# Optimization experiments

Hardware: AMD Instinct MI355X
Metric: run time of the kernel (lower is better)

The kernel has to match this reference:

```python
import jax, jax.numpy as jnp
import numpy as np

BN_INV = 1.0 / np.float32(np.sqrt(1.0 + 1e-5))  # eval BN with running_mean=0, running_var=1


def _conv(x, w, stride):
    return jax.lax.conv_general_dilated(
        x, w, (stride, stride), [(1, 1), (1, 1)],
        dimension_numbers=('NCHW', 'OIHW', 'NCHW'))


def _se(x, w1, b1, w2, b2):
    # squeeze-excite: global avg pool -> fc -> relu -> fc -> sigmoid -> scale
    y = x.mean(axis=(2, 3))                       # (B, C)
    y = jax.nn.relu(y @ w1.T + b1)
    y = jax.nn.sigmoid(y @ w2.T + b2)
    return x * y[:, :, None, None]


def _squash(s):
    n2 = jnp.sum(s * s, axis=-1, keepdims=True)
    n = jnp.sqrt(n2)
    return s * (n2 / (1.0 + n2)) / (n + 1e-8)


def _block(x, cw, g, b, s1w, s1b, s2w, s2b, stride):
    h = _conv(x, cw, stride)
    h = h * (g * BN_INV)[None, :, None, None] + b[None, :, None, None]
    h = jax.nn.relu(h)
    return _se(h, s1w, s1b, s2w, s2b)


def setup_inputs() -> dict:
    key = jax.random.key(0)
    ks = jax.random.split(key, 32)
    rn = lambda i, shape, s=1.0: s * jax.random.normal(ks[i], shape, dtype=jnp.float32)
    d = {}
    d['x'] = rn(0, (64, 1, 128, 128))
    # feature extractor
    d['conv1_w'] = rn(1, (16, 1, 3, 3), 0.3)
    d['bn1_g'] = 1.0 + rn(2, (16,), 0.1)
    d['bn1_b'] = rn(3, (16,), 0.1)
    d['se1_w1'] = rn(4, (1, 16), 0.2); d['se1_b1'] = rn(5, (1,), 0.1)
    d['se1_w2'] = rn(6, (16, 1), 0.2); d['se1_b2'] = rn(7, (16,), 0.1)
    d['conv2_w'] = rn(8, (32, 16, 3, 3), 0.1)
    d['bn2_g'] = 1.0 + rn(9, (32,), 0.1)
    d['bn2_b'] = rn(10, (32,), 0.1)
    d['se2_w1'] = rn(11, (2, 32), 0.2); d['se2_b1'] = rn(12, (2,), 0.1)
    d['se2_w2'] = rn(13, (32, 2), 0.2); d['se2_b2'] = rn(14, (32,), 0.1)
    d['conv3_w'] = rn(15, (64, 32, 3, 3), 0.07)
    d['bn3_g'] = 1.0 + rn(16, (64,), 0.1)
    d['bn3_b'] = rn(17, (64,), 0.1)
    d['se3_w1'] = rn(18, (4, 64), 0.15); d['se3_b1'] = rn(19, (4,), 0.1)
    d['se3_w2'] = rn(20, (64, 4), 0.15); d['se3_b2'] = rn(21, (64,), 0.1)
    # primary capsules conv: 64 -> 8 caps * 8 dim = 64 channels, stride 2
    d['pc_w'] = rn(22, (64, 64, 3, 3), 0.05)
    d['pc_b'] = rn(23, (64,), 0.05)
    # digit capsule transform: (1, 2048, 3, 16, 8)
    d['W_digit'] = 0.01 * jax.random.normal(ks[24], (1, 2048, 3, 16, 8), dtype=jnp.float32)
    return d


def reference(x, conv1_w, bn1_g, bn1_b, se1_w1, se1_b1, se1_w2, se1_b2,
              conv2_w, bn2_g, bn2_b, se2_w1, se2_b1, se2_w2, se2_b2,
              conv3_w, bn3_g, bn3_b, se3_w1, se3_b1, se3_w2, se3_b2,
              pc_w, pc_b, W_digit):
    h = _block(x, conv1_w, bn1_g, bn1_b, se1_w1, se1_b1, se1_w2, se1_b2, 1)
    h = _block(h, conv2_w, bn2_g, bn2_b, se2_w1, se2_b1, se2_w2, se2_b2, 2)
    h = _block(h, conv3_w, bn3_g, bn3_b, se3_w1, se3_b1, se3_w2, se3_b2, 2)
    # primary capsules: conv -> (B, 8 caps, 8 dim, 16*16) -> (B, 2048, 8)
    u = _conv(h, pc_w, 2) + pc_b[None, :, None, None]     # (B, 64, 16, 16)
    B = u.shape[0]
    u = u.reshape(B, 8, 8, -1).transpose(0, 1, 3, 2).reshape(B, -1, 8)
    u = _squash(u)                                        # (B, 2048, 8)
    # u_hat[b,i,c,d] = sum_e W[0,i,c,d,e] * u[b,i,e]  (avoids torch's W.repeat)
    u_hat = jnp.einsum('icde,bie->bicd', W_digit[0], u)   # (B, 2048, 3, 16)
    b_ij = jnp.zeros((B, u_hat.shape[1], u_hat.shape[2], 1), u_hat.dtype)
    v_j = None
    for _ in range(3):  # fixed routing iterations
        c_ij = jax.nn.softmax(b_ij, axis=2)
        s_j = jnp.sum(c_ij * u_hat, axis=1, keepdims=True)  # (B,1,3,16)
        v_j = _squash(s_j)
        b_ij = b_ij + jnp.sum(u_hat * v_j, axis=-1, keepdims=True)
    v = v_j[:, 0]                                          # (B, 3, 16)
    return jnp.sqrt(jnp.sum(v * v, axis=-1))               # (B, 3) class lengths
```

## Files before the change

### kernel.cpp

```cpp
#include <hip/hip_runtime.h>
#include <math.h>

#define BN_INV_F 0.9999950000374997f

__device__ __forceinline__ void gload_lds4(const float* g, float* l) {
    __builtin_amdgcn_global_load_lds(
        (const __attribute__((address_space(1))) void*)g,
        (__attribute__((address_space(3))) void*)l, 4, 0, 0);
}
__device__ __forceinline__ void gload_lds16(const float* g, float* l) {
    __builtin_amdgcn_global_load_lds(
        (const __attribute__((address_space(1))) void*)g,
        (__attribute__((address_space(3))) void*)l, 16, 0, 0);
}

__global__ __launch_bounds__(256) void wtrans_all_k(
    const float* __restrict__ w1, const float* __restrict__ w2,
    const float* __restrict__ w3, const float* __restrict__ wp,
    float* __restrict__ w1t, float* __restrict__ w2t,
    float* __restrict__ w3t, float* __restrict__ wpt)
{
    int i = blockIdx.x * 256 + threadIdx.x;
    if (i < 144) {
        int co = i % 16, k = i / 16;
        w1t[i] = w1[co * 9 + k];
    } else if (i < 4752) {
        int t = i - 144;
        int co = t % 32, rk = t / 32, cin = rk / 9, k = rk % 9;
        w2t[t] = w2[(co * 16 + cin) * 9 + k];
    } else if (i < 23184) {
        int t = i - 4752;
        int co = t % 64, rk = t / 64, cin = rk / 9, k = rk % 9;
        w3t[t] = w3[(co * 32 + cin) * 9 + k];
    } else if (i < 60048) {
        int t = i - 23184;
        int co = t % 64, rk = t / 64, cin = rk / 9, k = rk % 9;
        wpt[t] = wp[(co * 64 + cin) * 9 + k];
    }
}

template <int CIN, int CINB, int COUT, int COB, int HIN, int HOUT, int STRIDE,
          int TW, int ROWS_T, int PPT, int CB, int NTHREADS,
          bool BN_RELU, bool SE_SUM, int HSE_IN, int KSPLIT>
__device__ __forceinline__ void conv_body(
    const float* __restrict__ in, const float* __restrict__ wt,
    const float* __restrict__ gamma, const float* __restrict__ beta,
    float* __restrict__ out, size_t pstride,
    float* __restrict__ se_sum, const float* __restrict__ se_sums_in,
    const float* __restrict__ se_w1, const float* __restrict__ se_b1,
    const float* __restrict__ se_w2, const float* __restrict__ se_b2,
    float inv_spatial)
{
    constexpr int WIN = HIN, WOUT = HOUT;
    constexpr int TH = ROWS_T * PPT;
    constexpr int IH_T = (TH - 1) * STRIDE + 3;
    constexpr int NW = NTHREADS / 64;
    constexpr int NCHUNK = CINB / CB;
    constexpr int SEGS = (WIN >= 64) ? (WIN / 64) : 1;
    constexpr int PAIRS = (IH_T + 1) / 2;
    constexpr int NG = COUT / COB;
    constexpr int IHW = IH_T * WIN;
    constexpr int CHUNK_BYTES = CB * IHW * 4;
    constexpr bool FAST16 = (CHUNK_BYTES % 1024) == 0;
    constexpr int NISS = CHUNK_BYTES / 1024;
    static_assert(NTHREADS == TW * ROWS_T, "geometry");
    static_assert(TW == WOUT, "tile must span full output width");
    static_assert(CINB % CB == 0, "chunking");
    static_assert(WIN % 64 == 0 || WIN == 32, "stage width");

    const int b = blockIdx.z;
    const int gy = blockIdx.y;
    const int ty = blockIdx.x;
    const int tid = threadIdx.x;
    const int wo = tid % TW;
    const int rg = tid / TW;
    const int g = gy % NG;
    const int kk = gy / NG;
    const int cin0 = kk * CINB;

    __shared__ float in_t[2][CB * IH_T * WIN];
    __shared__ float scl[CIN];
    __shared__ float gl[COB], bl[COB];
    __shared__ float red[NW][COB];
    __shared__ float hid[HSE_IN > 0 ? HSE_IN : 1];

    const float* inb = in + (size_t)b * CIN * HIN * WIN;
    const int gr0 = ty * TH * STRIDE - 1;
    const int wos = wo * STRIDE;
    const int wvid = tid >> 6, lane = tid & 63;
    const bool interior = (gr0 >= 0) && (gr0 + IH_T <= HIN);

    auto stage = [&](int c, int buf) {
        const int cb0 = cin0 + c * CB;
        float* bb = &in_t[buf][0];
        if (FAST16 && interior) {
            for (int i = wvid; i < NISS; i += NW) {
                int fe = i * 256 + lane * 4;
                int ci = fe / IHW;
                int rem = fe - ci * IHW;
                int lr = rem / WIN;
                int lc = rem - lr * WIN;
                const float* gsrc = inb + (size_t)(cb0 + ci) * (HIN * WIN)
                                  + (size_t)(gr0 + lr) * WIN + lc;
                gload_lds16(gsrc, bb + i * 256);
            }
        } else if (WIN >= 64) {
            for (int r = wvid; r < CB * IH_T; r += NW) {
                int ci = r / IH_T, lr = r - ci * IH_T;
                int gr = gr0 + lr;
                float* ldst = bb + (ci * IH_T + lr) * WIN;
                if (gr >= 0 && gr < HIN) {
                    const float* gsrc = inb + (size_t)(cb0 + ci) * HIN * WIN + (size_t)gr * WIN;
#pragma unroll
                    for (int s = 0; s < SEGS; ++s)
                        gload_lds4(gsrc + s * 64 + lane, ldst + s * 64);
                } else {
#pragma unroll
                    for (int s = 0; s < SEGS; ++s) ldst[s * 64 + lane] = 0.0f;
                }
            }
        } else {
            for (int pz = wvid; pz < CB * PAIRS; pz += NW) {
                int ci = pz / PAIRS, q = pz - ci * PAIRS;
                int lr0 = q * 2;
                int nr = (lr0 + 1 < IH_T) ? 2 : 1;
                int grr = gr0 + lr0;
                float* ldst = bb + (ci * IH_T + lr0) * WIN;
                if (nr == 2 && grr >= 0 && grr + 1 < HIN) {
                    const float* gsrc = inb + (size_t)(cb0 + ci) * HIN * WIN + (size_t)grr * WIN + lane;
                    gload_lds4(gsrc, ldst);
                } else {
                    for (int e = lane; e < nr * WIN; e += 64) {
                        int rr = e / WIN, cc = e - rr * WIN;
                        int gr = grr + rr;
                        ldst[e] = (gr >= 0 && gr < HIN)
                            ? inb[(size_t)(cb0 + ci) * HIN * WIN + (size_t)gr * WIN + cc] : 0.0f;
                    }
                }
            }
        }
    };

    stage(0, 0);

    if (HSE_IN > 0) {
        if (tid < HSE_IN) {
            float a = se_b1[tid];
            for (int c = 0; c < CIN; ++c)
                a = fmaf(se_sums_in[b * CIN + c] * inv_spatial, se_w1[tid * CIN + c], a);
            hid[tid] = fmaxf(a, 0.0f);
        }
        __syncthreads();
        if (tid < CIN) {
            float a = se_b2[tid];
            for (int h = 0; h < HSE_IN; ++h)
                a = fmaf(hid[h], se_w2[tid * HSE_IN + h], a);
            scl[tid] = 1.0f / (1.0f + expf(-a));
        }
    } else {
        for (int t = tid; t < CIN; t += NTHREADS) scl[t] = 1.0f;
    }
    if (tid < COB) {
        int co = g * COB + tid;
        if (BN_RELU) {
            gl[tid] = gamma[co] * BN_INV_F;
            bl[tid] = beta[co];
        } else {
            gl[tid] = (kk == 0) ? gamma[co] : 0.0f;
        }
    }

    float acc[PPT][COB];
#pragma unroll
    for (int p = 0; p < PPT; ++p)
#pragma unroll
        for (int co = 0; co < COB; ++co) acc[p][co] = 0.0f;

    int cur = 0;
    for (int c = 0; c < NCHUNK; ++c) {
        asm volatile("s_waitcnt vmcnt(0)" ::: "memory");
        __syncthreads();
        if (c + 1 < NCHUNK) stage(c + 1, cur ^ 1);

        const float* bb = &in_t[cur][0];
#pragma unroll
        for (int ci = 0; ci < CB; ++ci) {
            const int cw = cin0 + c * CB + ci;
            const float sc = scl[cw];
            const float* wtap = wt + (size_t)cw * 9 * COUT + g * COB;
            const float* bb_ci = bb + ci * IH_T * WIN;
#pragma unroll
            for (int kh = 0; kh < 3; ++kh) {
#pragma unroll
                for (int kw = 0; kw < 3; ++kw) {
                    const float* wrow = wtap + (kh * 3 + kw) * COUT;
#pragma unroll
                    for (int p = 0; p < PPT; ++p) {
                        const float* row = bb_ci + ((rg + p * ROWS_T) * STRIDE + kh) * WIN;
                        int wi = wos + kw - 1;
                        float v;
                        if (kw == 0) {
                            v = row[wi < 0 ? 0 : wi];
                            if (wi < 0) v = 0.0f;
                        } else if (STRIDE == 1 && kw == 2) {
                            v = row[wi >= WIN ? WIN - 1 : wi];
                            if (wi >= WIN) v = 0.0f;
                        } else {
                            v = row[wi];
                        }
                        v *= sc;
#pragma unroll
                        for (int co = 0; co < COB; ++co)
                            acc[p][co] = fmaf(wrow[co], v, acc[p][co]);
                    }
                }
            }
        }
        cur ^= 1;
    }

    float tsum[COB];
#pragma unroll
    for (int co = 0; co < COB; ++co) tsum[co] = 0.0f;
    float* ob = out + (size_t)kk * pstride
              + ((size_t)b * COUT + (size_t)g * COB) * HOUT * WOUT;
#pragma unroll
    for (int p = 0; p < PPT; ++p) {
        const int ho = ty * TH + rg + p * ROWS_T;
#pragma unroll
        for (int co = 0; co < COB; ++co) {
            float v;
            if (BN_RELU)
                v = fmaxf(fmaf(acc[p][co], gl[co], bl[co]), 0.0f);
            else
                v = acc[p][co] + gl[co];
            ob[(size_t)co * HOUT * WOUT + ho * WOUT + wo] = v;
            tsum[co] += v;
        }
    }

    if (SE_SUM) {
#pragma unroll
        for (int co = 0; co < COB; ++co) {
            float v = tsum[co];
            for (int off = 32; off; off >>= 1) v += __shfl_down(v, off, 64);
            if (lane == 0) red[wvid][co] = v;
        }
        __syncthreads();
        if (tid < COB) {
            float v = 0.0f;
#pragma unroll
            for (int k = 0; k < NW; ++k) v += red[k][tid];
            atomicAdd(&se_sum[b * COUT + g * COB + tid], v);
        }
    }
}

template <int CIN, int CINB, int COUT, int WCO, int HIN, int HOUT, int STRIDE,
          int TW, int PPT, int CB, int NTHREADS,
          bool BN_RELU, bool SE_SUM, int HSE_IN, int KSPLIT>
__device__ __forceinline__ void conv_ws_body(
    const float* __restrict__ in, const float* __restrict__ wt,
    const float* __restrict__ gamma, const float* __restrict__ beta,
    float* __restrict__ out, size_t pstride,
    float* __restrict__ se_sum, const float* __restrict__ se_sums_in,
    const float* __restrict__ se_w1, const float* __restrict__ se_b1,
    const float* __restrict__ se_w2, const float* __restrict__ se_b2,
    float inv_spatial)
{
    constexpr int WIN = HIN, WOUT = HOUT;
    constexpr int NW = NTHREADS / 64;
    constexpr int WROWS = 64 / TW;
    constexpr int TH = WROWS * PPT;
    constexpr int IH_T = (TH - 1) * STRIDE + 3;
    constexpr int COBT = NW * WCO;
    constexpr int NG = COUT / COBT;
    constexpr int NCHUNK = CINB / CB;
    constexpr int SEGS = WIN / 64;
    constexpr int HALF = WIN / 2;
    constexpr int ROWS = CB * IH_T;
    constexpr int NPW = (ROWS / NW) * SEGS;
    static_assert(STRIDE == 2, "wave-split body is stride-2 only");
    static_assert(TW == WOUT, "tile spans full width");
    static_assert(CINB % CB == 0, "chunking");
    static_assert(WIN % 64 == 0, "stage width");
    static_assert(COUT % COBT == 0, "cout split");
    static_assert(ROWS % NW == 0, "uniform DMA count per wave");
    static_assert(NCHUNK >= 2, "pipeline depth");

    const int b = blockIdx.z;
    const int gy = blockIdx.y;
    const int ty = blockIdx.x;
    const int tid = threadIdx.x;
    const int lane = tid & 63;
    const int wvu = __builtin_amdgcn_readfirstlane(tid >> 6);
    const int wo = lane % TW;
    const int rl = lane / TW;
    const int g = gy % NG;
    const int kk = gy / NG;
    const int cin0 = kk * CINB;

    __shared__ float in_t[3][CB * IH_T * WIN];
    __shared__ float scl[CIN];
    __shared__ float gl[COBT], bl[COBT];
    __shared__ float red[NW][WCO];
    __shared__ float hid[HSE_IN > 0 ? HSE_IN : 1];

    const float* inb = in + (size_t)b * CIN * HIN * WIN;
    const int gr0 = ty * TH * STRIDE - 1;
    const bool interior = (gr0 >= 0) && (gr0 + IH_T <= HIN);

    auto stage = [&](int c, int buf) {
        const int cb0 = cin0 + c * CB;
        float* bb = &in_t[buf][0];
        if (interior) {
            for (int r = wvu; r < ROWS; r += NW) {
                int ci = r / IH_T, lr = r - ci * IH_T;
                const float* gsrc = inb + (size_t)(cb0 + ci) * HIN * WIN + (size_t)(gr0 + lr) * WIN;
                float* ldst = bb + r * WIN;
#pragma unroll
                for (int s = 0; s < SEGS; ++s) {
                    int p = s * 64 + lane;
                    int half = p / HALF;
                    int idx = p - half * HALF;
                    gload_lds4(gsrc + 2 * idx + half, ldst + s * 64);
                }
            }
        } else {
            for (int r = wvu; r < ROWS; r += NW) {
                int ci = r / IH_T, lr = r - ci * IH_T;
                int gr = gr0 + lr;
                float* ldst = bb + r * WIN;
                if (gr >= 0 && gr < HIN) {
                    const float* gsrc = inb + (size_t)(cb0 + ci) * HIN * WIN + (size_t)gr * WIN;
#pragma unroll
                    for (int s = 0; s < SEGS; ++s) {
                        int p = s * 64 + lane;
                        int half = p / HALF;
                        int idx = p - half * HALF;
                        gload_lds4(gsrc + 2 * idx + half, ldst + s * 64);
                    }
                } else {
#pragma unroll
                    for (int s = 0; s < SEGS; ++s) ldst[s * 64 + lane] = 0.0f;
                }
            }
        }
    };

    if (HSE_IN > 0) {
        if (tid < HSE_IN) {
            float a = se_b1[tid];
            for (int c = 0; c < CIN; ++c)
                a = fmaf(se_sums_in[b * CIN + c] * inv_spatial, se_w1[tid * CIN + c], a);
            hid[tid] = fmaxf(a, 0.0f);
        }
        __syncthreads();
        if (tid < CIN) {
            float a = se_b2[tid];
            for (int h = 0; h < HSE_IN; ++h)
                a = fmaf(hid[h], se_w2[tid * HSE_IN + h], a);
            scl[tid] = 1.0f / (1.0f + expf(-a));
        }
    } else {
        for (int t = tid; t < CIN; t += NTHREADS) scl[t] = 1.0f;
    }
    if (tid < COBT) {
        int co = g * COBT + tid;
        if (BN_RELU) {
            gl[tid] = gamma[co] * BN_INV_F;
            bl[tid] = beta[co];
        } else {
            gl[tid] = (kk == 0) ? gamma[co] : 0.0f;
        }
    }
    __syncthreads();

    stage(0, 0);
    stage(1, 1);

    float acc[PPT][WCO];
#pragma unroll
    for (int p = 0; p < PPT; ++p)
#pragma unroll
        for (int co = 0; co < WCO; ++co) acc[p][co] = 0.0f;

    for (int c = 0; c < NCHUNK; ++c) {
        if (interior) {
            if (c + 1 < NCHUNK)
                asm volatile("s_waitcnt vmcnt(%0)" :: "i"(NPW) : "memory");
            else
                asm volatile("s_waitcnt vmcnt(0)" ::: "memory");
        } else {
            asm volatile("s_waitcnt vmcnt(0) lgkmcnt(0)" ::: "memory");
        }
        __builtin_amdgcn_s_barrier();
        __builtin_amdgcn_sched_barrier(0);
        if (c + 2 < NCHUNK) stage(c + 2, (c + 2) % 3);

        const float* bb = &in_t[c % 3][0];
#pragma unroll
        for (int ci = 0; ci < CB; ++ci) {
            const int cw = cin0 + c * CB + ci;
            const float sc = scl[cw];
            const float* wtap = wt + (size_t)cw * 9 * COUT + g * COBT + wvu * WCO;
            const float* bb_ci = bb + ci * IH_T * WIN;
#pragma unroll
            for (int kh = 0; kh < 3; ++kh) {
                float iwv[PPT][3];
#pragma unroll
                for (int p = 0; p < PPT; ++p) {
                    const float* row = bb_ci + ((rl + p * WROWS) * STRIDE + kh) * WIN;
                    float e  = row[wo];
                    float om = row[HALF + ((wo == 0) ? 0 : wo - 1)];
                    if (wo == 0) om = 0.0f;
                    float op = row[HALF + wo];
                    iwv[p][0] = om * sc;
                    iwv[p][1] = e * sc;
                    iwv[p][2] = op * sc;
                }
#pragma unroll
                for (int kw = 0; kw < 3; ++kw) {
                    const float* wrow = wtap + (kh * 3 + kw) * COUT;
#pragma unroll
                    for (int p = 0; p < PPT; ++p) {
                        const float v = iwv[p][kw];
#pragma unroll
                        for (int co = 0; co < WCO; ++co)
                            acc[p][co] = fmaf(wrow[co], v, acc[p][co]);
                    }
                }
            }
        }
    }

    float tsum[WCO];
#pragma unroll
    for (int co = 0; co < WCO; ++co) tsum[co] = 0.0f;
    float* ob = out + (size_t)kk * pstride
              + ((size_t)b * COUT + (size_t)g * COBT + (size_t)wvu * WCO) * HOUT * WOUT;
#pragma unroll
    for (int p = 0; p < PPT; ++p) {
        const int ho = ty * TH + rl + p * WROWS;
#pragma unroll
        for (int co = 0; co < WCO; ++co) {
            float v;
            if (BN_RELU)
                v = fmaxf(fmaf(acc[p][co], gl[wvu * WCO + co], bl[wvu * WCO + co]), 0.0f);
            else
                v = acc[p][co] + gl[wvu * WCO + co];
            ob[(size_t)co * HOUT * WOUT + ho * WOUT + wo] = v;
            tsum[co] += v;
        }
    }

    if (SE_SUM) {
#pragma unroll
        for (int co = 0; co < WCO; ++co) {
            float v = tsum[co];
            for (int off = 32; off; off >>= 1) v += __shfl_down(v, off, 64);
            if (lane == 0) red[wvu][co] = v;
        }
        __syncthreads();
        if (lane < WCO)
            atomicAdd(&se_sum[b * COUT + g * COBT + wvu * WCO + lane], red[wvu][lane]);
    }
}

#define CONV_ARGS \
    const float* __restrict__ in, const float* __restrict__ wt, \
    const float* __restrict__ gamma, const float* __restrict__ beta, \
    float* __restrict__ out, size_t pstride, float* __restrict__ se_sum, \
    const float* __restrict__ se_sums_in, \
    const float* __restrict__ se_w1, const float* __restrict__ se_b1, \
    const float* __restrict__ se_w2, const float* __restrict__ se_b2, \
    float inv_spatial
#define CONV_PASS in, wt, gamma, beta, out, pstride, se_sum, se_sums_in, \
    se_w1, se_b1, se_w2, se_b2, inv_spatial

__global__ __launch_bounds__(256) void conv1_k(CONV_ARGS) {
    conv_body<1, 1, 16, 16, 128, 128, 1, 128, 2, 2, 1, 256, true, true, 0, 1>(CONV_PASS);
}
__global__ __launch_bounds__(256) void conv2_k(CONV_ARGS) {
    conv_ws_body<16, 16, 32, 8, 128, 64, 2, 64, 2, 4, 256, true, true, 1, 1>(CONV_PASS);
}
__global__ __launch_bounds__(256) void conv3_k(CONV_ARGS) {
    conv_ws_body<32, 32, 64, 16, 64, 32, 2, 32, 1, 8, 256, true, true, 2, 1>(CONV_PASS);
}
__global__ __launch_bounds__(256) void pc_k(CONV_ARGS) {
    conv_body<64, 16, 64, 16, 32, 16, 2, 16, 16, 1, 4, 256, false, false, 4, 4>(CONV_PASS);
}

__global__ __launch_bounds__(256) void squash_uhat_k(
    const float* __restrict__ up, size_t pstride,
    const float* __restrict__ W, float* __restrict__ u_hat)
{
    const int base = blockIdx.x * 256;
    const int tid = threadIdx.x;
    __shared__ float ush[256][8];

    {
        const int cap = base + tid;
        const int b = cap >> 11, i = cap & 2047;
        const int chi = i >> 8, spx = i & 255;
        const size_t off = ((size_t)(b * 64 + chi * 8)) * 256 + spx;
        float s[8];
        float n2 = 0.0f;
#pragma unroll
        for (int j = 0; j < 8; j++) {
            const size_t o = off + (size_t)j * 256;
            s[j] = (up[o] + up[o + pstride]) + (up[o + 2 * pstride] + up[o + 3 * pstride]);
            n2 = fmaf(s[j], s[j], n2);
        }
        const float n = sqrtf(n2);
        const float f = (n2 / (1.0f + n2)) / (n + 1e-8f);
#pragma unroll
        for (int j = 0; j < 8; j++) ush[tid][j] = s[j] * f;
    }
    __syncthreads();

    float* ob = u_hat + (size_t)base * 48;
#pragma unroll 4
    for (int k = 0; k < 48; ++k) {
        int o = tid + k * 256;
        int c = o / 48, cd = o % 48;
        int gi = (base + c) & 2047;
        const float* wp = W + (size_t)gi * 384 + cd * 8;
        float a = 0.0f;
#pragma unroll
        for (int e = 0; e < 8; e++) a = fmaf(wp[e], ush[c][e], a);
        ob[o] = a;
    }
}

template <int IT>
__global__ __launch_bounds__(256) void sweep_k(const float* __restrict__ u_hat,
                                               const float* __restrict__ s_hist,
                                               float* __restrict__ s_out)
{
    const int b = blockIdx.y;
    const int i = blockIdx.x * 256 + threadIdx.x;
    const int tid = threadIdx.x;
    __shared__ float vsh[IT > 0 ? IT : 1][48];
    __shared__ float fac[IT > 0 ? IT : 1][3];
    __shared__ float red[4][48];

    const float4* qp = (const float4*)(u_hat + ((size_t)b * 2048 + i) * 48);
    float uhv[48];
#pragma unroll
    for (int q = 0; q < 12; ++q) {
        float4 t = qp[q];
        uhv[q * 4 + 0] = t.x; uhv[q * 4 + 1] = t.y;
        uhv[q * 4 + 2] = t.z; uhv[q * 4 + 3] = t.w;
    }

    if (IT > 0) {
        if (tid < IT * 48) {
            int t = tid / 48, c = tid % 48;
            vsh[t][c] = s_hist[((size_t)t * 64 + b) * 48 + c];
        }
        __syncthreads();
        if (tid < IT * 3) {
            int t = tid / 3, j = tid % 3;
            float n2 = 0.0f;
            for (int d = 0; d < 16; ++d) { float s = vsh[t][j * 16 + d]; n2 = fmaf(s, s, n2); }
            float n = sqrtf(n2);
            fac[t][j] = (n2 / (1.0f + n2)) / (n + 1e-8f);
        }
        __syncthreads();
        if (tid < IT * 48) {
            int t = tid / 48, c = tid % 48;
            vsh[t][c] *= fac[t][c / 16];
        }
        __syncthreads();
    }

    float c0, c1, c2;
    if (IT == 0) {
        c0 = c1 = c2 = (1.0f / 3.0f);
    } else {
        float b0 = 0.0f, b1 = 0.0f, b2 = 0.0f;
#pragma unroll
        for (int t = 0; t < IT; ++t)
#pragma unroll
            for (int d = 0; d < 16; ++d) {
                b0 = fmaf(uhv[d],      vsh[t][d],      b0);
                b1 = fmaf(uhv[16 + d], vsh[t][16 + d], b1);
                b2 = fmaf(uhv[32 + d], vsh[t][32 + d], b2);
            }
        float m = fmaxf(b0, fmaxf(b1, b2));
        float e0 = expf(b0 - m), e1 = expf(b1 - m), e2 = expf(b2 - m);
        float inv = 1.0f / (e0 + e1 + e2);
        c0 = e0 * inv; c1 = e1 * inv; c2 = e2 * inv;
    }

    float sp[48];
#pragma unroll
    for (int d = 0; d < 16; ++d) {
        sp[d]      = c0 * uhv[d];
        sp[16 + d] = c1 * uhv[16 + d];
        sp[32 + d] = c2 * uhv[32 + d];
    }
    const int lane = tid & 63, wv = tid >> 6;
#pragma unroll
    for (int j = 0; j < 48; ++j) {
        float x = sp[j];
        for (int off = 32; off; off >>= 1) x += __shfl_down(x, off, 64);
        if (lane == 0) red[wv][j] = x;
    }
    __syncthreads();
    if (tid < 48) {
        float x = red[0][tid] + red[1][tid] + red[2][tid] + red[3][tid];
        atomicAdd(&s_out[(size_t)b * 48 + tid], x);
    }
}

__global__ __launch_bounds__(64) void route_out_k(const float* __restrict__ s2,
                                                  float* __restrict__ out)
{
    const int b = blockIdx.x;
    __shared__ float s[48];
    if (threadIdx.x < 48) s[threadIdx.x] = s2[(size_t)b * 48 + threadIdx.x];
    __syncthreads();
    if (threadIdx.x < 3) {
        int j = threadIdx.x;
        float n2 = 0.0f;
        for (int d = 0; d < 16; ++d) { float v = s[j * 16 + d]; n2 = fmaf(v, v, n2); }
        float n = sqrtf(n2);
        float fc = (n2 / (1.0f + n2)) / (n + 1e-8f);
        out[b * 3 + j] = fc * n;
    }
}

extern "C" void kernel_launch(void* const* d_in, const int* in_sizes, int n_in,
                              void* d_out, int out_size, void* d_ws, size_t ws_size,
                              hipStream_t stream)
{
    const float* x       = (const float*)d_in[0];
    const float* conv1_w = (const float*)d_in[1];
    const float* bn1_g   = (const float*)d_in[2];
    const float* bn1_b   = (const float*)d_in[3];
    const float* se1_w1  = (const float*)d_in[4];
    const float* se1_b1  = (const float*)d_in[5];
    const float* se1_w2  = (const float*)d_in[6];
    const float* se1_b2  = (const float*)d_in[7];
    const float* conv2_w = (const float*)d_in[8];
    const float* bn2_g   = (const float*)d_in[9];
    const float* bn2_b   = (const float*)d_in[10];
    const float* se2_w1  = (const float*)d_in[11];
    const float* se2_b1  = (const float*)d_in[12];
    const float* se2_w2  = (const float*)d_in[13];
    const float* se2_b2  = (const float*)d_in[14];
    const float* conv3_w = (const float*)d_in[15];
    const float* bn3_g   = (const float*)d_in[16];
    const float* bn3_b   = (const float*)d_in[17];
    const float* se3_w1  = (const float*)d_in[18];
    const float* se3_b1  = (const float*)d_in[19];
    const float* se3_w2  = (const float*)d_in[20];
    const float* se3_b2  = (const float*)d_in[21];
    const float* pc_w    = (const float*)d_in[22];
    const float* pc_b    = (const float*)d_in[23];
    const float* W_digit = (const float*)d_in[24];

    float* ws = (float*)d_ws;
    float* h1     = ws;
    float* h2     = ws + 16777216;
    float* h3     = ws;
    float* uparts = ws + 4194304;
    float* u_hat  = ws + 9437184;
    float* sums   = ws + 25165824;
    float* s1 = sums, *s2 = sums + 1024, *s3 = sums + 3072;
    float* s_buf  = sums + 7168;
    float* w1t    = ws + 25182272;
    float* w2t    = w1t + 144;
    float* w3t    = w2t + 4608;
    float* wpt    = w3t + 18432;

    hipMemsetAsync(sums, 0, 16448 * sizeof(float), stream);
    wtrans_all_k<<<235, 256, 0, stream>>>(conv1_w, conv2_w, conv3_w, pc_w,
                                          w1t, w2t, w3t, wpt);

    conv1_k<<<dim3(32, 1, 64), 256, 0, stream>>>(
        x, w1t, bn1_g, bn1_b, h1, 0, s1,
        nullptr, nullptr, nullptr, nullptr, nullptr, 0.0f);

    conv2_k<<<dim3(32, 1, 64), 256, 0, stream>>>(
        h1, w2t, bn2_g, bn2_b, h2, 0, s2,
        s1, se1_w1, se1_b1, se1_w2, se1_b2, 1.0f / 16384.0f);

    conv3_k<<<dim3(16, 1, 64), 256, 0, stream>>>(
        h2, w3t, bn3_g, bn3_b, h3, 0, s3,
        s2, se2_w1, se2_b1, se2_w2, se2_b2, 1.0f / 4096.0f);

    pc_k<<<dim3(1, 16, 64), 256, 0, stream>>>(
        h3, wpt, pc_b, nullptr, uparts, (size_t)1048576, nullptr,
        s3, se3_w1, se3_b1, se3_w2, se3_b2, 1.0f / 1024.0f);

    squash_uhat_k<<<512, 256, 0, stream>>>(uparts, (size_t)1048576, W_digit, u_hat);

    sweep_k<0><<<dim3(8, 64), 256, 0, stream>>>(u_hat, s_buf, s_buf + 0 * 64 * 48);
    sweep_k<1><<<dim3(8, 64), 256, 0, stream>>>(u_hat, s_buf, s_buf + 1 * 64 * 48);
    sweep_k<2><<<dim3(8, 64), 256, 0, stream>>>(u_hat, s_buf, s_buf + 2 * 64 * 48);
    route_out_k<<<64, 64, 0, stream>>>(s_buf + 2 * 64 * 48, (float*)d_out);
}
```

Before: 224.6 us.

## Compute two adjacent output columns per thread in stride-2 conv2/conv3

Each thread now computes two horizontally adjacent output pixels instead of stacked rows. This lets the overlapping input tap (odd column) be shared between them and lets the kernel use float2 LDS reads and float2 global stores. Conv3 is retiled with fewer output channels per wave and a two-group channel split, which changes the grid shape to keep parallelism. The trade-off is different register pressure and a taller tile per block, which means more staged input rows.

```diff
diff --git a/kernel.cpp b/kernel.cpp
--- a/kernel.cpp
+++ b/kernel.cpp
@@ -256,22 +256,23 @@
     }
 }
 
-template <int CIN, int CINB, int COUT, int WCO, int HIN, int HOUT, int STRIDE,
-          int TW, int PPT, int CB, int NTHREADS,
-          bool BN_RELU, bool SE_SUM, int HSE_IN, int KSPLIT>
-__device__ __forceinline__ void conv_ws_body(
+template <int CIN, int CINB, int COUT, int WCO, int HIN, int HOUT,
+          int TW, int CB, int NTHREADS,
+          bool BN_RELU, bool SE_SUM, int HSE_IN>
+__device__ __forceinline__ void conv_ws2_body(
     const float* __restrict__ in, const float* __restrict__ wt,
     const float* __restrict__ gamma, const float* __restrict__ beta,
-    float* __restrict__ out, size_t pstride,
+    float* __restrict__ out,
     float* __restrict__ se_sum, const float* __restrict__ se_sums_in,
     const float* __restrict__ se_w1, const float* __restrict__ se_b1,
     const float* __restrict__ se_w2, const float* __restrict__ se_b2,
     float inv_spatial)
 {
     constexpr int WIN = HIN, WOUT = HOUT;
+    constexpr int STRIDE = 2;
     constexpr int NW = NTHREADS / 64;
-    constexpr int WROWS = 64 / TW;
-    constexpr int TH = WROWS * PPT;
+    constexpr int NP = TW / 2;
+    constexpr int TH = 64 / NP;
     constexpr int IH_T = (TH - 1) * STRIDE + 3;
     constexpr int COBT = NW * WCO;
     constexpr int NG = COUT / COBT;
@@ -280,7 +281,6 @@
     constexpr int HALF = WIN / 2;
     constexpr int ROWS = CB * IH_T;
     constexpr int NPW = (ROWS / NW) * SEGS;
-    static_assert(STRIDE == 2, "wave-split body is stride-2 only");
     static_assert(TW == WOUT, "tile spans full width");
     static_assert(CINB % CB == 0, "chunking");
     static_assert(WIN % 64 == 0, "stage width");
@@ -294,8 +294,8 @@
     const int tid = threadIdx.x;
     const int lane = tid & 63;
     const int wvu = __builtin_amdgcn_readfirstlane(tid >> 6);
-    const int wo = lane % TW;
-    const int rl = lane / TW;
+    const int wo2 = lane % NP;
+    const int rl = lane / NP;
     const int g = gy % NG;
     const int kk = gy / NG;
     const int cin0 = kk * CINB;
@@ -379,11 +379,9 @@
     stage(0, 0);
     stage(1, 1);
 
-    float acc[PPT][WCO];
-#pragma unroll
-    for (int p = 0; p < PPT; ++p)
-#pragma unroll
-        for (int co = 0; co < WCO; ++co) acc[p][co] = 0.0f;
+    float acc0[WCO], acc1[WCO];
+#pragma unroll
+    for (int co = 0; co < WCO; ++co) { acc0[co] = 0.0f; acc1[co] = 0.0f; }
 
     for (int c = 0; c < NCHUNK; ++c) {
         if (interior) {
@@ -407,28 +405,27 @@
             const float* bb_ci = bb + ci * IH_T * WIN;
 #pragma unroll
             for (int kh = 0; kh < 3; ++kh) {
-                float iwv[PPT][3];
-#pragma unroll
-                for (int p = 0; p < PPT; ++p) {
-                    const float* row = bb_ci + ((rl + p * WROWS) * STRIDE + kh) * WIN;
-                    float e  = row[wo];
-                    float om = row[HALF + ((wo == 0) ? 0 : wo - 1)];
-                    if (wo == 0) om = 0.0f;
-                    float op = row[HALF + wo];
-                    iwv[p][0] = om * sc;
-                    iwv[p][1] = e * sc;
-                    iwv[p][2] = op * sc;
-                }
-#pragma unroll
-                for (int kw = 0; kw < 3; ++kw) {
-                    const float* wrow = wtap + (kh * 3 + kw) * COUT;
-#pragma unroll
-                    for (int p = 0; p < PPT; ++p) {
-                        const float v = iwv[p][kw];
-#pragma unroll
-                        for (int co = 0; co < WCO; ++co)
-                            acc[p][co] = fmaf(wrow[co], v, acc[p][co]);
-                    }
+                const float* row = bb_ci + (rl * STRIDE + kh) * WIN;
+                float2 E2 = *(const float2*)(row + 2 * wo2);
+                float2 O2 = *(const float2*)(row + HALF + 2 * wo2);
+                float om = row[HALF + ((wo2 == 0) ? 0 : (2 * wo2 - 1))];
+                if (wo2 == 0) om = 0.0f;
+                const float vm0 = om   * sc;
+                const float ve0 = E2.x * sc;
+                const float vp0 = O2.x * sc;
+                const float ve1 = E2.y * sc;
+                const float vp1 = O2.y * sc;
+                const float* w0 = wtap + (kh * 3 + 0) * COUT;
+                const float* w1 = wtap + (kh * 3 + 1) * COUT;
+                const float* w2 = wtap + (kh * 3 + 2) * COUT;
+#pragma unroll
+                for (int co = 0; co < WCO; ++co) {
+                    acc0[co] = fmaf(w0[co], vm0, acc0[co]);
+                    acc0[co] = fmaf(w1[co], ve0, acc0[co]);
+                    acc0[co] = fmaf(w2[co], vp0, acc0[co]);
+                    acc1[co] = fmaf(w0[co], vp0, acc1[co]);
+                    acc1[co] = fmaf(w1[co], ve1, acc1[co]);
+                    acc1[co] = fmaf(w2[co], vp1, acc1[co]);
                 }
             }
         }
@@ -437,21 +434,23 @@
     float tsum[WCO];
 #pragma unroll
     for (int co = 0; co < WCO; ++co) tsum[co] = 0.0f;
-    float* ob = out + (size_t)kk * pstride
-              + ((size_t)b * COUT + (size_t)g * COBT + (size_t)wvu * WCO) * HOUT * WOUT;
-#pragma unroll
-    for (int p = 0; p < PPT; ++p) {
-        const int ho = ty * TH + rl + p * WROWS;
-#pragma unroll
-        for (int co = 0; co < WCO; ++co) {
-            float v;
-            if (BN_RELU)
-                v = fmaxf(fmaf(acc[p][co], gl[wvu * WCO + co], bl[wvu * WCO + co]), 0.0f);
-            else
-                v = acc[p][co] + gl[wvu * WCO + co];
-            ob[(size_t)co * HOUT * WOUT + ho * WOUT + wo] = v;
-            tsum[co] += v;
-        }
+    const int ho = ty * TH + rl;
+    float* ob = out + ((size_t)b * COUT + (size_t)g * COBT + (size_t)wvu * WCO) * HOUT * WOUT;
+#pragma unroll
+    for (int co = 0; co < WCO; ++co) {
+        float v0, v1;
+        const float gg = gl[wvu * WCO + co];
+        if (BN_RELU) {
+            const float bb2 = bl[wvu * WCO + co];
+            v0 = fmaxf(fmaf(acc0[co], gg, bb2), 0.0f);
+            v1 = fmaxf(fmaf(acc1[co], gg, bb2), 0.0f);
+        } else {
+            v0 = acc0[co] + gg;
+            v1 = acc1[co] + gg;
+        }
+        float2 vv; vv.x = v0; vv.y = v1;
+        *(float2*)(ob + (size_t)co * HOUT * WOUT + (size_t)ho * WOUT + 2 * wo2) = vv;
+        tsum[co] += v0 + v1;
     }
 
     if (SE_SUM) {
@@ -477,15 +476,17 @@
     float inv_spatial
 #define CONV_PASS in, wt, gamma, beta, out, pstride, se_sum, se_sums_in, \
     se_w1, se_b1, se_w2, se_b2, inv_spatial
+#define CONV_PASS2 in, wt, gamma, beta, out, se_sum, se_sums_in, \
+    se_w1, se_b1, se_w2, se_b2, inv_spatial
 
 __global__ __launch_bounds__(256) void conv1_k(CONV_ARGS) {
     conv_body<1, 1, 16, 16, 128, 128, 1, 128, 2, 2, 1, 256, true, true, 0, 1>(CONV_PASS);
 }
 __global__ __launch_bounds__(256) void conv2_k(CONV_ARGS) {
-    conv_ws_body<16, 16, 32, 8, 128, 64, 2, 64, 2, 4, 256, true, true, 1, 1>(CONV_PASS);
+    conv_ws2_body<16, 16, 32, 8, 128, 64, 64, 4, 256, true, true, 1>(CONV_PASS2);
 }
 __global__ __launch_bounds__(256) void conv3_k(CONV_ARGS) {
-    conv_ws_body<32, 32, 64, 16, 64, 32, 2, 32, 1, 8, 256, true, true, 2, 1>(CONV_PASS);
+    conv_ws2_body<32, 32, 64, 8, 64, 32, 32, 4, 256, true, true, 2>(CONV_PASS2);
 }
 __global__ __launch_bounds__(256) void pc_k(CONV_ARGS) {
     conv_body<64, 16, 64, 16, 32, 16, 2, 16, 16, 1, 4, 256, false, false, 4, 4>(CONV_PASS);
@@ -688,7 +689,7 @@
         h1, w2t, bn2_g, bn2_b, h2, 0, s2,
         s1, se1_w1, se1_b1, se1_w2, se1_b2, 1.0f / 16384.0f);
 
-    conv3_k<<<dim3(16, 1, 64), 256, 0, stream>>>(
+    conv3_k<<<dim3(8, 2, 64), 256, 0, stream>>>(
         h2, w3t, bn3_g, bn3_b, h3, 0, s3,
         s2, se2_w1, se2_b1, se2_w2, se2_b2, 1.0f / 4096.0f);
 
```

Measured after the change: 212.5 us. -5.4%, faster.
